# Optimization experiments

Measured on AMD Instinct MI355X. Metric: run time of the kernel, lower is better.

Reference implementation:

```python
import jax, jax.numpy as jnp
import numpy as np

DEPTH = 3
HEADS = 8
DIM = 512
MLP = 4096
NUM_CLASS = 4
EPS = 1e-5
SCALE = (DIM // HEADS) ** -0.5


def _layernorm(x, g, b):
    mu = jnp.mean(x, axis=-1, keepdims=True)
    var = jnp.mean(jnp.square(x - mu), axis=-1, keepdims=True)
    return (x - mu) * jax.lax.rsqrt(var + EPS) * g + b


def setup_inputs() -> dict:
    key = jax.random.key(0)
    ks = jax.random.split(key, 16)
    B, N = 2, 2560
    s = 0.02
    inp = {
        "x": jax.random.normal(ks[0], (B, N, DIM), jnp.float32),
        "mask": jax.random.randint(ks[1], (B, NUM_CLASS), 0, 2, jnp.int32),
        # per-layer params stacked on leading depth axis
        "ln1_g": jnp.ones((DEPTH, DIM), jnp.float32),
        "ln1_b": jnp.zeros((DEPTH, DIM), jnp.float32),
        "qkv_w": jax.random.normal(ks[2], (DEPTH, DIM, 3 * DIM), jnp.float32) * s,  # qkv_bias=False
        "proj_w": jax.random.normal(ks[3], (DEPTH, DIM, DIM), jnp.float32) * s,
        "proj_b": jnp.zeros((DEPTH, DIM), jnp.float32),
        "ln2_g": jnp.ones((DEPTH, DIM), jnp.float32),
        "ln2_b": jnp.zeros((DEPTH, DIM), jnp.float32),
        "ffn_w1": jax.random.normal(ks[4], (DEPTH, DIM, MLP), jnp.float32) * s,
        "ffn_b1": jnp.zeros((DEPTH, MLP), jnp.float32),
        "ffn_w2": jax.random.normal(ks[5], (DEPTH, MLP, DIM), jnp.float32) * s,
        "ffn_b2": jnp.zeros((DEPTH, DIM), jnp.float32),
    }
    return inp


def reference(x, mask, ln1_g, ln1_b, qkv_w, proj_w, proj_b, ln2_g, ln2_b,
              ffn_w1, ffn_b1, ffn_w2, ffn_b2):
    B, N, C = x.shape
    n = N // (NUM_CLASS + 1)  # tokens per modality block
    # mask_gen_fusion: columns of missing-modality blocks are masked out;
    # fusion block (last n tokens) is always attendable.
    avail = jnp.concatenate(
        [jnp.repeat(mask.astype(bool), n, axis=1), jnp.ones((B, n), bool)], axis=1)  # [B, N]
    neg_inf = jnp.asarray(-jnp.inf, x.dtype)

    attn_list = []
    for j in range(DEPTH):
        # --- masked attention block (Residual(PreNormDrop(MaskedAttention))) ---
        h = _layernorm(x, ln1_g[j], ln1_b[j])
        qkv = (h @ qkv_w[j]).reshape(B, N, 3, HEADS, C // HEADS)
        q, k, v = (qkv[:, :, i].transpose(0, 2, 1, 3) for i in range(3))  # [B,H,N,hd]
        attn = jnp.einsum("bhqd,bhkd->bhqk", q, k) * SCALE
        attn = jnp.where(avail[:, None, None, :], attn, neg_inf)
        attn = jax.nn.softmax(attn, axis=-1)
        o = jnp.einsum("bhqk,bhkd->bhqd", attn, v).transpose(0, 2, 1, 3).reshape(B, N, C)
        x = x + (o @ proj_w[j] + proj_b[j])  # dropout = identity (eval)
        attn_list.append(attn)
        # --- FFN block (Residual(PreNorm(FeedForward))) ---
        h = _layernorm(x, ln2_g[j], ln2_b[j])
        h = jax.nn.gelu(h @ ffn_w1[j] + ffn_b1[j]) @ ffn_w2[j] + ffn_b2[j]
        x = x + h
    return x, jnp.stack(attn_list, axis=0)  # [depth,B,H,N,N]
```

## Files before the change

kernel.cpp:

```cpp
#include <hip/hip_runtime.h>
#include <math.h>

#define DEPTH 3
#define HEADS 8
#define DIM 512
#define NCLS 4
#define EPSV 1e-5f
#define BB 2
#define NN 2560
#define HD 64
#define ATT_SCALE 0.125f

typedef __attribute__((ext_vector_type(8))) short bf16x8;
typedef __attribute__((ext_vector_type(4))) float f32x4;

__device__ inline unsigned short bf16_rne(float f) {
    unsigned int u = __float_as_uint(f);
    u += 0x7FFFu + ((u >> 16) & 1u);
    return (unsigned short)(u >> 16);
}
__device__ inline float bf16_tof(unsigned short h) {
    return __uint_as_float(((unsigned int)h) << 16);
}
__device__ inline void split2(float f, unsigned short& hi, unsigned short& lo) {
    hi = bf16_rne(f);
    lo = bf16_rne(f - bf16_tof(hi));
}

__device__ inline float gelu_tanh(float x) {
    float x3 = x * x * x;
    return 0.5f * x * (1.f + tanhf(0.7978845608028654f * (x + 0.044715f * x3)));
}

__device__ inline int swz(int row, int chunk) { return chunk ^ ((row >> 1) & 3); }

__device__ inline void gll16(const void* g, void* l) {
    __builtin_amdgcn_global_load_lds(
        (const __attribute__((address_space(1))) void*)g,
        (__attribute__((address_space(3))) void*)l,
        16, 0, 0);
}

template<int ROWS>
__device__ inline void stage_plane(const unsigned short* gp, int ldp,
                                   unsigned short* ls, int lane, int wave) {
#pragma unroll
    for (int q = 0; q < ROWS / 64; ++q) {
        int base = wave * (ROWS * 16) + q * 1024;
        int lpos = base + lane * 16;
        int row  = lpos >> 6;
        int cl   = (lpos >> 4) & 3;
        int cg   = swz(row, cl);
        gll16(gp + (size_t)row * ldp + cg * 8, (char*)ls + base);
    }
}

__device__ inline void stage_a_f32(const float* ga, int lda,
                                   unsigned short* lhi, unsigned short* llo, int tid) {
    int row = tid >> 1, half = tid & 1;
    const float* src = ga + (size_t)row * lda + half * 16;
#pragma unroll
    for (int c2 = 0; c2 < 2; ++c2) {
        float4 p0 = *(const float4*)(src + c2 * 8);
        float4 p1 = *(const float4*)(src + c2 * 8 + 4);
        float v[8] = {p0.x, p0.y, p0.z, p0.w, p1.x, p1.y, p1.z, p1.w};
        bf16x8 hv, lv;
#pragma unroll
        for (int i = 0; i < 8; ++i) {
            unsigned short h, l;
            split2(v[i], h, l);
            hv[i] = (short)h; lv[i] = (short)l;
        }
        int chunk = half * 2 + c2;
        int idx = row * 32 + swz(row, chunk) * 8;
        *(bf16x8*)&lhi[idx] = hv;
        *(bf16x8*)&llo[idx] = lv;
    }
}

template<int BN, bool A_F32, bool DO_GELU, bool DO_RESID, bool SPLIT_OUT, bool ZSWZ>
__global__ __launch_bounds__(256, (BN == 128 ? 2 : 3)) void gemm_mfma(
    const float* __restrict__ Af,
    const unsigned short* __restrict__ A_hi, const unsigned short* __restrict__ A_lo,
    int lda, long long sAb, long long sAh,
    const unsigned short* __restrict__ B_hi, const unsigned short* __restrict__ B_lo,
    int ldb, long long sBb, long long sBh,
    float* __restrict__ Cf,
    unsigned short* __restrict__ C_hi, unsigned short* __restrict__ C_lo,
    int ldc, long long sCb, long long sCh,
    int K, float alpha, const float* __restrict__ bias, int nh)
{
    constexpr int BM = 128;
    constexpr int WAVES_N = (BN == 128) ? 2 : 1;
    constexpr int WM = (WAVES_N == 2) ? 64 : 32;
    constexpr int WN = 64;
    constexpr int MF = WM / 16;
    constexpr int NF = WN / 16;

    __shared__ unsigned short As_hi[BM * 32], As_lo[BM * 32];
    __shared__ unsigned short Bs_hi[BN * 32], Bs_lo[BN * 32];

    int bx = blockIdx.x, by = blockIdx.y, bzz = blockIdx.z;
    if constexpr (ZSWZ) {
        int gx = gridDim.x, gy = gridDim.y, gz = gridDim.z;
        int pb = gx * gy;
        int total = pb * gz;
        int flat = bx + gx * (by + gy * bzz);
        int cpx = total >> 3;
        int nf = (flat & 7) * cpx + (flat >> 3);
        bzz = nf / pb;
        int r = nf - bzz * pb;
        by = r / gx;
        bx = r - by * gx;
    }

    const int bz = bzz / nh, hz = bzz % nh;
    const long long aoff = (long long)bz * sAb + (long long)hz * sAh;
    const long long boff = (long long)bz * sBb + (long long)hz * sBh;
    const long long coff = (long long)bz * sCb + (long long)hz * sCh;
    if (A_F32) { Af += aoff; } else { A_hi += aoff; A_lo += aoff; }
    B_hi += boff; B_lo += boff;
    if (SPLIT_OUT) { C_hi += coff; C_lo += coff; } else { Cf += coff; }

    const int tid  = threadIdx.x;
    const int lane = tid & 63;
    const int wave = tid >> 6;
    const int row0 = by * BM;
    const int n0   = bx * BN;
    const int wr = (WAVES_N == 2) ? (wave >> 1) : wave;
    const int wc = (WAVES_N == 2) ? (wave & 1) : 0;
    const int lr = lane & 15;
    const int cg = lane >> 4;

    f32x4 acc[MF][NF];
#pragma unroll
    for (int m = 0; m < MF; ++m)
#pragma unroll
        for (int n = 0; n < NF; ++n)
#pragma unroll
            for (int i = 0; i < 4; ++i) acc[m][n][i] = 0.f;

    for (int k0 = 0; k0 < K; k0 += 32) {
        if constexpr (A_F32) {
            stage_a_f32(Af + (size_t)row0 * lda + k0, lda, As_hi, As_lo, tid);
        } else {
            stage_plane<BM>(A_hi + (size_t)row0 * lda + k0, lda, As_hi, lane, wave);
            stage_plane<BM>(A_lo + (size_t)row0 * lda + k0, lda, As_lo, lane, wave);
        }
        stage_plane<BN>(B_hi + (size_t)n0 * ldb + k0, ldb, Bs_hi, lane, wave);
        stage_plane<BN>(B_lo + (size_t)n0 * ldb + k0, ldb, Bs_lo, lane, wave);
        __syncthreads();

        bf16x8 ah[MF], al[MF], bh[NF], bl[NF];
#pragma unroll
        for (int m = 0; m < MF; ++m) {
            int r = wr * WM + m * 16 + lr;
            int idx = r * 32 + swz(r, cg) * 8;
            ah[m] = *(const bf16x8*)&As_hi[idx];
            al[m] = *(const bf16x8*)&As_lo[idx];
        }
#pragma unroll
        for (int n = 0; n < NF; ++n) {
            int r = wc * WN + n * 16 + lr;
            int idx = r * 32 + swz(r, cg) * 8;
            bh[n] = *(const bf16x8*)&Bs_hi[idx];
            bl[n] = *(const bf16x8*)&Bs_lo[idx];
        }
#pragma unroll
        for (int m = 0; m < MF; ++m)
#pragma unroll
            for (int n = 0; n < NF; ++n) {
                acc[m][n] = __builtin_amdgcn_mfma_f32_16x16x32_bf16(ah[m], bh[n], acc[m][n], 0, 0, 0);
                acc[m][n] = __builtin_amdgcn_mfma_f32_16x16x32_bf16(ah[m], bl[n], acc[m][n], 0, 0, 0);
                acc[m][n] = __builtin_amdgcn_mfma_f32_16x16x32_bf16(al[m], bh[n], acc[m][n], 0, 0, 0);
            }
        __syncthreads();
    }

    float bv[NF];
#pragma unroll
    for (int n = 0; n < NF; ++n) {
        int col = n0 + wc * WN + n * 16 + lr;
        bv[n] = bias ? bias[col] : 0.f;
    }
#pragma unroll
    for (int m = 0; m < MF; ++m) {
#pragma unroll
        for (int n = 0; n < NF; ++n) {
            int col = n0 + wc * WN + n * 16 + lr;
#pragma unroll
            for (int i = 0; i < 4; ++i) {
                int row = row0 + wr * WM + m * 16 + cg * 4 + i;
                size_t off = (size_t)row * ldc + col;
                float r = alpha * acc[m][n][i] + bv[n];
                if constexpr (DO_GELU) r = gelu_tanh(r);
                if constexpr (SPLIT_OUT) {
                    unsigned short h, l;
                    split2(r, h, l);
                    C_hi[off] = h; C_lo[off] = l;
                } else {
                    if constexpr (DO_RESID) r += Cf[off];
                    Cf[off] = r;
                }
            }
        }
    }
}

__global__ __launch_bounds__(256) void ln_split_kernel(const float* __restrict__ x,
                                                       const float* __restrict__ g,
                                                       const float* __restrict__ b,
                                                       unsigned short* __restrict__ ohi,
                                                       unsigned short* __restrict__ olo) {
    int wave = threadIdx.x >> 6;
    int lane = threadIdx.x & 63;
    int row  = blockIdx.x * 4 + wave;
    const float* xr = x + (size_t)row * DIM;
    float v[8];
    float s = 0.f, ss = 0.f;
#pragma unroll
    for (int i = 0; i < 8; ++i) {
        v[i] = xr[lane + i * 64];
        s += v[i]; ss += v[i] * v[i];
    }
#pragma unroll
    for (int off = 32; off >= 1; off >>= 1) {
        s  += __shfl_xor(s,  off, 64);
        ss += __shfl_xor(ss, off, 64);
    }
    float mu   = s * (1.f / DIM);
    float var  = ss * (1.f / DIM) - mu * mu;
    float rstd = rsqrtf(var + EPSV);
    size_t base = (size_t)row * DIM;
#pragma unroll
    for (int i = 0; i < 8; ++i) {
        int c = lane + i * 64;
        float r = (v[i] - mu) * rstd * g[c] + b[c];
        unsigned short h, l;
        split2(r, h, l);
        ohi[base + c] = h; olo[base + c] = l;
    }
}

__global__ __launch_bounds__(256) void tsplit_kernel(
    const float* __restrict__ in, int ldin, long long inBS,
    unsigned short* __restrict__ ohi, unsigned short* __restrict__ olo,
    int ldout, long long outBS) {
    __shared__ float tile[32][33];
    const float* src = in + (size_t)blockIdx.z * inBS;
    int r0 = blockIdx.y * 32, c0 = blockIdx.x * 32;
    int t = threadIdx.x;
    int r = t >> 3, cq = (t & 7) * 4;
    float4 v = *(const float4*)&src[(size_t)(r0 + r) * ldin + c0 + cq];
    tile[r][cq] = v.x; tile[r][cq + 1] = v.y; tile[r][cq + 2] = v.z; tile[r][cq + 3] = v.w;
    __syncthreads();
    unsigned short h[4], l[4];
#pragma unroll
    for (int i = 0; i < 4; ++i) split2(tile[cq + i][r], h[i], l[i]);
    size_t off = (size_t)blockIdx.z * outBS + (size_t)(c0 + r) * ldout + r0 + cq;
    *(ushort4*)&ohi[off] = make_ushort4(h[0], h[1], h[2], h[3]);
    *(ushort4*)&olo[off] = make_ushort4(l[0], l[1], l[2], l[3]);
}

__global__ __launch_bounds__(256) void softmax_kernel(float* __restrict__ attn,
                                                      const int* __restrict__ mask) {
    int q = blockIdx.x, h = blockIdx.y, b = blockIdx.z;
    float* row = attn + (((size_t)(b * HEADS + h)) * NN + q) * NN;
    int t = threadIdx.x;

    float v[10];
    bool ok[10];
    float lmax = -INFINITY;
#pragma unroll
    for (int i = 0; i < 10; ++i) {
        int col = t + i * 256;
        int cls = col >> 9;
        ok[i] = (cls >= NCLS) || (mask[b * NCLS + cls] != 0);
        v[i] = row[col];
        if (ok[i]) lmax = fmaxf(lmax, v[i]);
    }
    __shared__ float red[4];
#pragma unroll
    for (int off = 32; off >= 1; off >>= 1) lmax = fmaxf(lmax, __shfl_xor(lmax, off, 64));
    if ((t & 63) == 0) red[t >> 6] = lmax;
    __syncthreads();
    float m = fmaxf(fmaxf(red[0], red[1]), fmaxf(red[2], red[3]));
    __syncthreads();

    float lsum = 0.f;
#pragma unroll
    for (int i = 0; i < 10; ++i) {
        if (ok[i]) { v[i] = __expf(v[i] - m); lsum += v[i]; }
    }
#pragma unroll
    for (int off = 32; off >= 1; off >>= 1) lsum += __shfl_xor(lsum, off, 64);
    if ((t & 63) == 0) red[t >> 6] = lsum;
    __syncthreads();
    float inv = 1.f / (red[0] + red[1] + red[2] + red[3]);

#pragma unroll
    for (int i = 0; i < 10; ++i) {
        int col = t + i * 256;
        row[col] = ok[i] ? v[i] * inv : 0.f;
    }
}

extern "C" void kernel_launch(void* const* d_in, const int* in_sizes, int n_in,
                              void* d_out, int out_size, void* d_ws, size_t ws_size,
                              hipStream_t stream) {
    (void)in_sizes; (void)n_in; (void)out_size; (void)ws_size;
    const float* x_in   = (const float*)d_in[0];
    const int*   mask   = (const int*)d_in[1];
    const float* ln1_g  = (const float*)d_in[2];
    const float* ln1_b  = (const float*)d_in[3];
    const float* qkv_w  = (const float*)d_in[4];
    const float* proj_w = (const float*)d_in[5];
    const float* proj_b = (const float*)d_in[6];
    const float* ln2_g  = (const float*)d_in[7];
    const float* ln2_b  = (const float*)d_in[8];
    const float* ffn_w1 = (const float*)d_in[9];
    const float* ffn_b1 = (const float*)d_in[10];
    const float* ffn_w2 = (const float*)d_in[11];
    const float* ffn_b2 = (const float*)d_in[12];

    const size_t xsz = (size_t)BB * NN * DIM;
    float* xbuf     = (float*)d_out;
    float* attn_all = (float*)d_out + xsz;

    unsigned short* Wq_hi = (unsigned short*)d_ws;
    unsigned short* Wq_lo = Wq_hi + (size_t)1536 * 512;
    unsigned short* Wp_hi = Wq_lo + (size_t)1536 * 512;
    unsigned short* Wp_lo = Wp_hi + (size_t)512 * 512;
    unsigned short* W1_hi = Wp_lo + (size_t)512 * 512;
    unsigned short* W1_lo = W1_hi + (size_t)4096 * 512;
    unsigned short* W2_hi = W1_lo + (size_t)4096 * 512;
    unsigned short* W2_lo = W2_hi + (size_t)4096 * 512;
    unsigned short* h_hi  = W2_lo + (size_t)4096 * 512;
    unsigned short* h_lo  = h_hi + xsz;
    unsigned short* U     = h_lo + xsz;
    unsigned short* qk_hi = U;
    unsigned short* qk_lo = qk_hi + (size_t)5120 * 1024;
    float*          Vf    = (float*)(qk_lo + (size_t)5120 * 1024);
    unsigned short* vt_hi = (unsigned short*)(Vf + xsz);
    unsigned short* vt_lo = vt_hi + (size_t)2 * 512 * 2560;
    unsigned short* o_hi  = vt_lo + (size_t)2 * 512 * 2560;
    unsigned short* o_lo  = o_hi + xsz;
    unsigned short* g_hi  = U;
    unsigned short* g_lo  = g_hi + (size_t)5120 * 4096;

    hipMemcpyAsync(xbuf, x_in, xsz * sizeof(float), hipMemcpyDeviceToDevice, stream);

    dim3 blk(256);
    const int M = BB * NN;

    for (int j = 0; j < DEPTH; ++j) {
        tsplit_kernel<<<dim3(1536 / 32, 512 / 32, 1), blk, 0, stream>>>(
            qkv_w + (size_t)j * 512 * 1536, 1536, 0, Wq_hi, Wq_lo, 512, 0);
        tsplit_kernel<<<dim3(512 / 32, 512 / 32, 1), blk, 0, stream>>>(
            proj_w + (size_t)j * 512 * 512, 512, 0, Wp_hi, Wp_lo, 512, 0);
        tsplit_kernel<<<dim3(4096 / 32, 512 / 32, 1), blk, 0, stream>>>(
            ffn_w1 + (size_t)j * 512 * 4096, 4096, 0, W1_hi, W1_lo, 512, 0);
        tsplit_kernel<<<dim3(512 / 32, 4096 / 32, 1), blk, 0, stream>>>(
            ffn_w2 + (size_t)j * 4096 * 512, 512, 0, W2_hi, W2_lo, 4096, 0);

        ln_split_kernel<<<dim3(M / 4), blk, 0, stream>>>(xbuf, ln1_g + j * DIM, ln1_b + j * DIM, h_hi, h_lo);

        gemm_mfma<128, false, false, false, true, true><<<dim3(8, 40, 1), blk, 0, stream>>>(
            nullptr, h_hi, h_lo, DIM, 0, 0,
            Wq_hi, Wq_lo, DIM, 0, 0,
            nullptr, qk_hi, qk_lo, 1024, 0, 0,
            DIM, 1.f, nullptr, 1);
        gemm_mfma<64, false, false, false, false, true><<<dim3(8, 40, 1), blk, 0, stream>>>(
            nullptr, h_hi, h_lo, DIM, 0, 0,
            Wq_hi + (size_t)1024 * 512, Wq_lo + (size_t)1024 * 512, DIM, 0, 0,
            Vf, nullptr, nullptr, DIM, 0, 0,
            DIM, 1.f, nullptr, 1);
        tsplit_kernel<<<dim3(512 / 32, 2560 / 32, BB), blk, 0, stream>>>(
            Vf, DIM, (long long)NN * DIM, vt_hi, vt_lo, NN, (long long)DIM * NN);

        float* attn_j = attn_all + (size_t)j * BB * HEADS * NN * NN;
        gemm_mfma<128, false, false, false, false, true><<<dim3(20, 20, BB * HEADS), blk, 0, stream>>>(
            nullptr, qk_hi, qk_lo, 1024, (long long)NN * 1024, HD,
            qk_hi + 512, qk_lo + 512, 1024, (long long)NN * 1024, HD,
            attn_j, nullptr, nullptr, NN, (long long)HEADS * NN * NN, (long long)NN * NN,
            HD, ATT_SCALE, nullptr, HEADS);

        softmax_kernel<<<dim3(NN, HEADS, BB), blk, 0, stream>>>(attn_j, mask);

        gemm_mfma<64, true, false, false, true, true><<<dim3(1, 20, BB * HEADS), blk, 0, stream>>>(
            attn_j, nullptr, nullptr, NN, (long long)HEADS * NN * NN, (long long)NN * NN,
            vt_hi, vt_lo, NN, (long long)DIM * NN, (long long)HD * NN,
            nullptr, o_hi, o_lo, DIM, (long long)NN * DIM, HD,
            NN, 1.f, nullptr, HEADS);

        gemm_mfma<64, false, false, true, false, true><<<dim3(8, 40, 1), blk, 0, stream>>>(
            nullptr, o_hi, o_lo, DIM, 0, 0,
            Wp_hi, Wp_lo, DIM, 0, 0,
            xbuf, nullptr, nullptr, DIM, 0, 0,
            DIM, 1.f, proj_b + j * DIM, 1);

        ln_split_kernel<<<dim3(M / 4), blk, 0, stream>>>(xbuf, ln2_g + j * DIM, ln2_b + j * DIM, h_hi, h_lo);

        gemm_mfma<128, false, true, false, true, true><<<dim3(32, 40, 1), blk, 0, stream>>>(
            nullptr, h_hi, h_lo, DIM, 0, 0,
            W1_hi, W1_lo, DIM, 0, 0,
            nullptr, g_hi, g_lo, 4096, 0, 0,
            DIM, 1.f, ffn_b1 + (size_t)j * 4096, 1);

        gemm_mfma<64, false, false, true, false, true><<<dim3(8, 40, 1), blk, 0, stream>>>(
            nullptr, g_hi, g_lo, 4096, 0, 0,
            W2_hi, W2_lo, 4096, 0, 0,
            xbuf, nullptr, nullptr, DIM, 0, 0,
            4096, 1.f, ffn_b2 + j * DIM, 1);
    }
}
```

Measured before the change: 3.229 ms.

## Fuse softmax with PV product and add split-K atomics to projection GEMMs

The separate softmax kernel and the attention-times-V GEMM are replaced by one kernel. It normalises each block of 8 query rows, writes the probabilities back to the attention output, and keeps a bf16 copy in shared memory to feed the MFMA PV product. This avoids re-reading the full fp32 attention matrix and re-splitting it into hi/lo planes. The projection and FFN2 GEMMs are also split along K, with atomicAdd into the residual buffer, to launch more blocks. In exchange, the probability operand drops the lo-plane correction term, and atomic accumulation makes the order of floating-point sums nondeterministic.

```diff
diff --git a/kernel.cpp b/kernel.cpp
--- a/kernel.cpp
+++ b/kernel.cpp
@@ -10,6 +10,7 @@
 #define NN 2560
 #define HD 64
 #define ATT_SCALE 0.125f
+#define QB 8
 
 typedef __attribute__((ext_vector_type(8))) short bf16x8;
 typedef __attribute__((ext_vector_type(4))) float f32x4;
@@ -55,32 +56,8 @@
     }
 }
 
-__device__ inline void stage_a_f32(const float* ga, int lda,
-                                   unsigned short* lhi, unsigned short* llo, int tid) {
-    int row = tid >> 1, half = tid & 1;
-    const float* src = ga + (size_t)row * lda + half * 16;
-#pragma unroll
-    for (int c2 = 0; c2 < 2; ++c2) {
-        float4 p0 = *(const float4*)(src + c2 * 8);
-        float4 p1 = *(const float4*)(src + c2 * 8 + 4);
-        float v[8] = {p0.x, p0.y, p0.z, p0.w, p1.x, p1.y, p1.z, p1.w};
-        bf16x8 hv, lv;
-#pragma unroll
-        for (int i = 0; i < 8; ++i) {
-            unsigned short h, l;
-            split2(v[i], h, l);
-            hv[i] = (short)h; lv[i] = (short)l;
-        }
-        int chunk = half * 2 + c2;
-        int idx = row * 32 + swz(row, chunk) * 8;
-        *(bf16x8*)&lhi[idx] = hv;
-        *(bf16x8*)&llo[idx] = lv;
-    }
-}
-
-template<int BN, bool A_F32, bool DO_GELU, bool DO_RESID, bool SPLIT_OUT, bool ZSWZ>
+template<int BN, bool DO_GELU, bool DO_RESID, bool SPLIT_OUT, bool ZSWZ, int SPLITK>
 __global__ __launch_bounds__(256, (BN == 128 ? 2 : 3)) void gemm_mfma(
-    const float* __restrict__ Af,
     const unsigned short* __restrict__ A_hi, const unsigned short* __restrict__ A_lo,
     int lda, long long sAb, long long sAh,
     const unsigned short* __restrict__ B_hi, const unsigned short* __restrict__ B_lo,
@@ -114,11 +91,14 @@
         bx = r - by * gx;
     }
 
+    int kz = 0;
+    if constexpr (SPLITK > 1) { kz = bzz; bzz = 0; }
+
     const int bz = bzz / nh, hz = bzz % nh;
     const long long aoff = (long long)bz * sAb + (long long)hz * sAh;
     const long long boff = (long long)bz * sBb + (long long)hz * sBh;
     const long long coff = (long long)bz * sCb + (long long)hz * sCh;
-    if (A_F32) { Af += aoff; } else { A_hi += aoff; A_lo += aoff; }
+    A_hi += aoff; A_lo += aoff;
     B_hi += boff; B_lo += boff;
     if (SPLIT_OUT) { C_hi += coff; C_lo += coff; } else { Cf += coff; }
 
@@ -140,13 +120,11 @@
 #pragma unroll
             for (int i = 0; i < 4; ++i) acc[m][n][i] = 0.f;
 
-    for (int k0 = 0; k0 < K; k0 += 32) {
-        if constexpr (A_F32) {
-            stage_a_f32(Af + (size_t)row0 * lda + k0, lda, As_hi, As_lo, tid);
-        } else {
-            stage_plane<BM>(A_hi + (size_t)row0 * lda + k0, lda, As_hi, lane, wave);
-            stage_plane<BM>(A_lo + (size_t)row0 * lda + k0, lda, As_lo, lane, wave);
-        }
+    const int kb = kz * (K / SPLITK);
+    const int ke = kb + K / SPLITK;
+    for (int k0 = kb; k0 < ke; k0 += 32) {
+        stage_plane<BM>(A_hi + (size_t)row0 * lda + k0, lda, As_hi, lane, wave);
+        stage_plane<BM>(A_lo + (size_t)row0 * lda + k0, lda, As_lo, lane, wave);
         stage_plane<BN>(B_hi + (size_t)n0 * ldb + k0, ldb, Bs_hi, lane, wave);
         stage_plane<BN>(B_lo + (size_t)n0 * ldb + k0, ldb, Bs_lo, lane, wave);
         __syncthreads();
@@ -181,7 +159,7 @@
 #pragma unroll
     for (int n = 0; n < NF; ++n) {
         int col = n0 + wc * WN + n * 16 + lr;
-        bv[n] = bias ? bias[col] : 0.f;
+        bv[n] = (bias && kz == 0) ? bias[col] : 0.f;
     }
 #pragma unroll
     for (int m = 0; m < MF; ++m) {
@@ -194,7 +172,9 @@
                 size_t off = (size_t)row * ldc + col;
                 float r = alpha * acc[m][n][i] + bv[n];
                 if constexpr (DO_GELU) r = gelu_tanh(r);
-                if constexpr (SPLIT_OUT) {
+                if constexpr (SPLITK > 1) {
+                    atomicAdd(&Cf[off], r);
+                } else if constexpr (SPLIT_OUT) {
                     unsigned short h, l;
                     split2(r, h, l);
                     C_hi[off] = h; C_lo[off] = l;
@@ -262,46 +242,115 @@
     *(ushort4*)&olo[off] = make_ushort4(l[0], l[1], l[2], l[3]);
 }
 
-__global__ __launch_bounds__(256) void softmax_kernel(float* __restrict__ attn,
-                                                      const int* __restrict__ mask) {
-    int q = blockIdx.x, h = blockIdx.y, b = blockIdx.z;
-    float* row = attn + (((size_t)(b * HEADS + h)) * NN + q) * NN;
-    int t = threadIdx.x;
-
-    float v[10];
-    bool ok[10];
-    float lmax = -INFINITY;
-#pragma unroll
-    for (int i = 0; i < 10; ++i) {
-        int col = t + i * 256;
-        int cls = col >> 9;
-        ok[i] = (cls >= NCLS) || (mask[b * NCLS + cls] != 0);
-        v[i] = row[col];
-        if (ok[i]) lmax = fmaxf(lmax, v[i]);
-    }
-    __shared__ float red[4];
-#pragma unroll
-    for (int off = 32; off >= 1; off >>= 1) lmax = fmaxf(lmax, __shfl_xor(lmax, off, 64));
-    if ((t & 63) == 0) red[t >> 6] = lmax;
+__global__ __launch_bounds__(256) void softmax_pv_kernel(
+    float* __restrict__ attn, const int* __restrict__ mask,
+    const unsigned short* __restrict__ vt_hi, const unsigned short* __restrict__ vt_lo,
+    unsigned short* __restrict__ o_hi, unsigned short* __restrict__ o_lo)
+{
+    __shared__ unsigned short P[QB * NN];
+    __shared__ float Ored[4][QB * 64];
+
+    const int qb = blockIdx.x, h = blockIdx.y, b = blockIdx.z;
+    const int q0 = qb * QB;
+    const int tid = threadIdx.x, lane = tid & 63, wave = tid >> 6;
+    float* base = attn + (((size_t)(b * HEADS + h)) * NN + q0) * NN;
+
+    bool mok[NCLS];
+#pragma unroll
+    for (int c = 0; c < NCLS; ++c) mok[c] = (mask[b * NCLS + c] != 0);
+
+    for (int rr = 0; rr < 2; ++rr) {
+        int row = wave * 2 + rr;
+        float* rp = base + (size_t)row * NN;
+        float4 v[10];
+        bool okv[10];
+        float lmax = -INFINITY;
+#pragma unroll
+        for (int i = 0; i < 10; ++i) {
+            int k4 = lane + 64 * i;
+            v[i] = *(const float4*)&rp[4 * k4];
+            int cls = k4 >> 7;
+            okv[i] = (cls >= NCLS) || mok[cls];
+            if (okv[i]) lmax = fmaxf(lmax,
+                fmaxf(fmaxf(v[i].x, v[i].y), fmaxf(v[i].z, v[i].w)));
+        }
+#pragma unroll
+        for (int off = 32; off >= 1; off >>= 1) lmax = fmaxf(lmax, __shfl_xor(lmax, off, 64));
+        float lsum = 0.f;
+#pragma unroll
+        for (int i = 0; i < 10; ++i) {
+            if (okv[i]) {
+                v[i].x = __expf(v[i].x - lmax); v[i].y = __expf(v[i].y - lmax);
+                v[i].z = __expf(v[i].z - lmax); v[i].w = __expf(v[i].w - lmax);
+                lsum += v[i].x + v[i].y + v[i].z + v[i].w;
+            } else {
+                v[i] = make_float4(0.f, 0.f, 0.f, 0.f);
+            }
+        }
+#pragma unroll
+        for (int off = 32; off >= 1; off >>= 1) lsum += __shfl_xor(lsum, off, 64);
+        float inv = 1.f / lsum;
+#pragma unroll
+        for (int i = 0; i < 10; ++i) {
+            int k4 = lane + 64 * i;
+            float4 p = make_float4(v[i].x * inv, v[i].y * inv, v[i].z * inv, v[i].w * inv);
+            *(float4*)&rp[4 * k4] = p;
+            int c = k4 >> 1, sub = k4 & 1;
+            int cp = c ^ (row & 7);
+            ushort4 pk = make_ushort4(bf16_rne(p.x), bf16_rne(p.y), bf16_rne(p.z), bf16_rne(p.w));
+            *(ushort4*)&P[row * NN + cp * 8 + sub * 4] = pk;
+        }
+    }
     __syncthreads();
-    float m = fmaxf(fmaxf(red[0], red[1]), fmaxf(red[2], red[3]));
+
+    const int lr = lane & 15;
+    const int cg = lane >> 4;
+    const unsigned short* vbh = vt_hi + (size_t)b * DIM * NN + (size_t)(h * HD) * NN;
+    const unsigned short* vbl = vt_lo + (size_t)b * DIM * NN + (size_t)(h * HD) * NN;
+
+    f32x4 acc[4];
+#pragma unroll
+    for (int n = 0; n < 4; ++n)
+#pragma unroll
+        for (int i = 0; i < 4; ++i) acc[n][i] = 0.f;
+
+    const bf16x8 az = {0, 0, 0, 0, 0, 0, 0, 0};
+#pragma unroll 2
+    for (int t = 0; t < NN / (4 * 32); ++t) {
+        int k0 = wave * (NN / 4) + t * 32;
+        bf16x8 ah = az;
+        if (lr < QB) ah = *(const bf16x8*)&P[lr * NN + (((k0 >> 3) + cg) ^ lr) * 8];
+        bf16x8 bh[4], bl[4];
+#pragma unroll
+        for (int n = 0; n < 4; ++n) {
+            size_t doff = (size_t)(n * 16 + lr) * NN + k0 + cg * 8;
+            bh[n] = *(const bf16x8*)&vbh[doff];
+            bl[n] = *(const bf16x8*)&vbl[doff];
+        }
+#pragma unroll
+        for (int n = 0; n < 4; ++n) {
+            acc[n] = __builtin_amdgcn_mfma_f32_16x16x32_bf16(ah, bh[n], acc[n], 0, 0, 0);
+            acc[n] = __builtin_amdgcn_mfma_f32_16x16x32_bf16(ah, bl[n], acc[n], 0, 0, 0);
+        }
+    }
+
+    if (cg < 2) {
+#pragma unroll
+        for (int n = 0; n < 4; ++n)
+#pragma unroll
+            for (int i = 0; i < 4; ++i)
+                Ored[wave][(cg * 4 + i) * 64 + n * 16 + lr] = acc[n][i];
+    }
     __syncthreads();
 
-    float lsum = 0.f;
-#pragma unroll
-    for (int i = 0; i < 10; ++i) {
-        if (ok[i]) { v[i] = __expf(v[i] - m); lsum += v[i]; }
-    }
-#pragma unroll
-    for (int off = 32; off >= 1; off >>= 1) lsum += __shfl_xor(lsum, off, 64);
-    if ((t & 63) == 0) red[t >> 6] = lsum;
-    __syncthreads();
-    float inv = 1.f / (red[0] + red[1] + red[2] + red[3]);
-
-#pragma unroll
-    for (int i = 0; i < 10; ++i) {
-        int col = t + i * 256;
-        row[col] = ok[i] ? v[i] * inv : 0.f;
+#pragma unroll
+    for (int e = tid; e < QB * 64; e += 256) {
+        float s = Ored[0][e] + Ored[1][e] + Ored[2][e] + Ored[3][e];
+        int r = e >> 6, c = e & 63;
+        unsigned short hh, ll;
+        split2(s, hh, ll);
+        size_t off = (size_t)(b * NN + q0 + r) * DIM + h * HD + c;
+        o_hi[off] = hh; o_lo[off] = ll;
     }
 }
 
@@ -365,13 +414,13 @@
 
         ln_split_kernel<<<dim3(M / 4), blk, 0, stream>>>(xbuf, ln1_g + j * DIM, ln1_b + j * DIM, h_hi, h_lo);
 
-        gemm_mfma<128, false, false, false, true, true><<<dim3(8, 40, 1), blk, 0, stream>>>(
-            nullptr, h_hi, h_lo, DIM, 0, 0,
+        gemm_mfma<128, false, false, true, true, 1><<<dim3(8, 40, 1), blk, 0, stream>>>(
+            h_hi, h_lo, DIM, 0, 0,
             Wq_hi, Wq_lo, DIM, 0, 0,
             nullptr, qk_hi, qk_lo, 1024, 0, 0,
             DIM, 1.f, nullptr, 1);
-        gemm_mfma<64, false, false, false, false, true><<<dim3(8, 40, 1), blk, 0, stream>>>(
-            nullptr, h_hi, h_lo, DIM, 0, 0,
+        gemm_mfma<64, false, false, false, true, 1><<<dim3(8, 40, 1), blk, 0, stream>>>(
+            h_hi, h_lo, DIM, 0, 0,
             Wq_hi + (size_t)1024 * 512, Wq_lo + (size_t)1024 * 512, DIM, 0, 0,
             Vf, nullptr, nullptr, DIM, 0, 0,
             DIM, 1.f, nullptr, 1);
@@ -379,36 +428,31 @@
             Vf, DIM, (long long)NN * DIM, vt_hi, vt_lo, NN, (long long)DIM * NN);
 
         float* attn_j = attn_all + (size_t)j * BB * HEADS * NN * NN;
-        gemm_mfma<128, false, false, false, false, true><<<dim3(20, 20, BB * HEADS), blk, 0, stream>>>(
-            nullptr, qk_hi, qk_lo, 1024, (long long)NN * 1024, HD,
+        gemm_mfma<128, false, false, false, true, 1><<<dim3(20, 20, BB * HEADS), blk, 0, stream>>>(
+            qk_hi, qk_lo, 1024, (long long)NN * 1024, HD,
             qk_hi + 512, qk_lo + 512, 1024, (long long)NN * 1024, HD,
             attn_j, nullptr, nullptr, NN, (long long)HEADS * NN * NN, (long long)NN * NN,
             HD, ATT_SCALE, nullptr, HEADS);
 
-        softmax_kernel<<<dim3(NN, HEADS, BB), blk, 0, stream>>>(attn_j, mask);
-
-        gemm_mfma<64, true, false, false, true, true><<<dim3(1, 20, BB * HEADS), blk, 0, stream>>>(
-            attn_j, nullptr, nullptr, NN, (long long)HEADS * NN * NN, (long long)NN * NN,
-            vt_hi, vt_lo, NN, (long long)DIM * NN, (long long)HD * NN,
-            nullptr, o_hi, o_lo, DIM, (long long)NN * DIM, HD,
-            NN, 1.f, nullptr, HEADS);
-
-        gemm_mfma<64, false, false, true, false, true><<<dim3(8, 40, 1), blk, 0, stream>>>(
-            nullptr, o_hi, o_lo, DIM, 0, 0,
+        softmax_pv_kernel<<<dim3(NN / QB, HEADS, BB), blk, 0, stream>>>(
+            attn_j, mask, vt_hi, vt_lo, o_hi, o_lo);
+
+        gemm_mfma<64, false, true, false, true, 2><<<dim3(8, 40, 2), blk, 0, stream>>>(
+            o_hi, o_lo, DIM, 0, 0,
             Wp_hi, Wp_lo, DIM, 0, 0,
             xbuf, nullptr, nullptr, DIM, 0, 0,
             DIM, 1.f, proj_b + j * DIM, 1);
 
         ln_split_kernel<<<dim3(M / 4), blk, 0, stream>>>(xbuf, ln2_g + j * DIM, ln2_b + j * DIM, h_hi, h_lo);
 
-        gemm_mfma<128, false, true, false, true, true><<<dim3(32, 40, 1), blk, 0, stream>>>(
-            nullptr, h_hi, h_lo, DIM, 0, 0,
+        gemm_mfma<128, true, false, true, true, 1><<<dim3(32, 40, 1), blk, 0, stream>>>(
+            h_hi, h_lo, DIM, 0, 0,
             W1_hi, W1_lo, DIM, 0, 0,
             nullptr, g_hi, g_lo, 4096, 0, 0,
             DIM, 1.f, ffn_b1 + (size_t)j * 4096, 1);
 
-        gemm_mfma<64, false, false, true, false, true><<<dim3(8, 40, 1), blk, 0, stream>>>(
-            nullptr, g_hi, g_lo, 4096, 0, 0,
+        gemm_mfma<64, false, true, false, true, 4><<<dim3(8, 40, 4), blk, 0, stream>>>(
+            g_hi, g_lo, 4096, 0, 0,
             W2_hi, W2_lo, 4096, 0, 0,
             xbuf, nullptr, nullptr, DIM, 0, 0,
             4096, 1.f, ffn_b2 + j * DIM, 1);
```

After: 3.793 ms. 17.5% more time.
